# Optimization experiments

Measured on AMD Instinct MI355X. Metric: run time of the kernel, lower is better.

The kernel has to match this reference:

```python
import jax, jax.numpy as jnp
import numpy as np

THRESHOLD = 0.1  # matches init kwarg 'threshold'


def setup_inputs() -> dict:
    key = jax.random.key(0)
    ks = jax.random.split(key, 4)
    B, T, D = 16, 4096, 1024   # batch, tokens(=patch_h*patch_w), d_model
    E, R = 8, 64               # experts, lora rank
    inputs = jax.random.normal(ks[0], (B, T, D), dtype=jnp.float32)
    gate_w = jax.random.normal(ks[1], (D, E), dtype=jnp.float32) * (1.0 / np.sqrt(D))
    gate_b = jnp.zeros((E,), dtype=jnp.float32)
    lora_A = jax.random.normal(ks[2], (E, D, R), dtype=jnp.float32) * (1.0 / np.sqrt(D))
    lora_B = jax.random.normal(ks[3], (E, R, D), dtype=jnp.float32) * (1.0 / np.sqrt(R))
    return {"inputs": inputs, "gate_w": gate_w, "gate_b": gate_b,
            "lora_A": lora_A, "lora_B": lora_B, "patch_h": 64, "patch_w": 64}


def reference(inputs, gate_w, gate_b, lora_A, lora_B, patch_h, patch_w):
    # patch_h / patch_w are unused by 'linear' LoRA experts (kept for signature parity)
    D = inputs.shape[-1]
    x = inputs.reshape(-1, D)                                  # [N, D]
    gate_logits = jax.nn.softmax(x @ gate_w + gate_b, axis=-1)  # [N, E]
    selected = (gate_logits >= THRESHOLD).astype(x.dtype)       # threshold gate
    weights = gate_logits * selected
    wsum = jnp.sum(weights, axis=-1, keepdims=True)
    wsum = jnp.where(wsum == 0, jnp.ones_like(wsum), wsum)
    weights = weights / wsum                                    # renormalized weights [N, E]
    # Dense equivalent of per-expert gather/scatter: tokens with weight 0 contribute nothing,
    # identical to the boolean-indexed accumulation in the torch code.
    h = jnp.einsum('nd,edr->ner', x, lora_A)                    # [N, E, R]
    out = jnp.einsum('ner,erd,ne->nd', h, lora_B, weights)      # weighted combine [N, D]
    return out.reshape(inputs.shape[:-1] + (D,))
```

## Files before the change

kernel.cpp:

```cpp
#include <hip/hip_runtime.h>
#include <stdint.h>
#include <stddef.h>


typedef float f32x4 __attribute__((ext_vector_type(4)));
typedef short bf16x8 __attribute__((ext_vector_type(8)));

#define MFMA_16x16x32(A, B, C) __builtin_amdgcn_mfma_f32_16x16x32_bf16((A), (B), (C), 0, 0, 0)
#define SCHED_FENCE() __builtin_amdgcn_sched_barrier(0)
#define BAR() __builtin_amdgcn_s_barrier()
#define WAIT_LGKM0() asm volatile("s_waitcnt lgkmcnt(0)" ::: "memory")
#define WAIT_VM3() asm volatile("s_waitcnt vmcnt(3)" ::: "memory")
#define WAIT_VM0_LGKM0() asm volatile("s_waitcnt vmcnt(0) lgkmcnt(0)" ::: "memory")
#define WAIT_VM0() asm volatile("s_waitcnt vmcnt(0)" ::: "memory")

__device__ __forceinline__ unsigned short f2bf(float f) {
    union { float f; unsigned int u; } v;
    v.f = f;
    unsigned int u = v.u;
    u += 0x7FFFu + ((u >> 16) & 1u);
    return (unsigned short)(u >> 16);
}

__device__ __forceinline__ void load16_lds(unsigned short* lds, const unsigned short* g) {
    __builtin_amdgcn_global_load_lds(
        (const __attribute__((address_space(1))) unsigned int*)g,
        (__attribute__((address_space(3))) unsigned int*)lds, 16, 0, 0);
}

__global__ __launch_bounds__(256) void convert_pack(
        const float* __restrict__ LA, const float* __restrict__ LB,
        unsigned short* __restrict__ A_P, unsigned short* __restrict__ B_P) {
    int gid = blockIdx.x * 256 + threadIdx.x;
    if (gid < 524288) {
        int j = gid & 7, l = (gid >> 3) & 63, cblk = (gid >> 9) & 31, kblk = gid >> 14;
        int d = kblk * 32 + (l >> 4) * 8 + j;
        int col = cblk * 16 + (l & 15);
        int e = col >> 6, r = col & 63;
        A_P[gid] = f2bf(LA[((size_t)e * 1024 + d) * 64 + r]);
    } else {
        int idx = gid - 524288;
        int j = idx & 7, l = (idx >> 3) & 63, cblk = (idx >> 9) & 63, kblk = idx >> 15;
        int k = kblk * 32 + (l >> 4) * 8 + j;
        int d = cblk * 16 + (l & 15);
        int e = k >> 6, r = k & 63;
        B_P[idx] = f2bf(LB[((size_t)e * 64 + r) * 1024 + d]);
    }
}

__global__ __launch_bounds__(256) void gate_kernel(
        const float* __restrict__ X, const float* __restrict__ GW,
        const float* __restrict__ GB, float* __restrict__ Wg) {
    __shared__ float gwt[8 * 1024];
    int tid = threadIdx.x;

    {
        float r[4][8];
#pragma unroll
        for (int j = 0; j < 4; ++j) {
            const f32x4* gp = (const f32x4*)(GW + (size_t)(tid * 4 + j) * 8);
            f32x4 g0 = gp[0], g1 = gp[1];
#pragma unroll
            for (int q = 0; q < 4; ++q) { r[j][q] = g0[q]; r[j][4 + q] = g1[q]; }
        }
#pragma unroll
        for (int e = 0; e < 8; ++e) {
            f32x4 v;
#pragma unroll
            for (int j = 0; j < 4; ++j) v[j] = r[j][e];
            *(f32x4*)&gwt[e * 1024 + tid * 4] = v;
        }
    }
    __syncthreads();

    int tg = tid >> 4;
    int sub = tid & 15;
    size_t tok0 = (size_t)blockIdx.x * 64 + tg * 4;
    const float* xr = X + tok0 * 1024 + sub * 4;

    float lg[4][8];
#pragma unroll
    for (int ti = 0; ti < 4; ++ti)
#pragma unroll
        for (int e = 0; e < 8; ++e) lg[ti][e] = 0.f;

#pragma unroll 2
    for (int it = 0; it < 16; ++it) {
        f32x4 g[8];
#pragma unroll
        for (int e = 0; e < 8; ++e)
            g[e] = *(const f32x4*)&gwt[e * 1024 + it * 64 + sub * 4];
#pragma unroll
        for (int ti = 0; ti < 4; ++ti) {
            f32x4 x = *(const f32x4*)(xr + (size_t)ti * 1024 + it * 64);
#pragma unroll
            for (int e = 0; e < 8; ++e) {
                lg[ti][e] += x[0] * g[e][0];
                lg[ti][e] += x[1] * g[e][1];
                lg[ti][e] += x[2] * g[e][2];
                lg[ti][e] += x[3] * g[e][3];
            }
        }
    }
#pragma unroll
    for (int s = 1; s < 16; s <<= 1) {
#pragma unroll
        for (int ti = 0; ti < 4; ++ti)
#pragma unroll
            for (int e = 0; e < 8; ++e)
                lg[ti][e] += __shfl_xor(lg[ti][e], s, 16);
    }
#pragma unroll
    for (int ti = 0; ti < 4; ++ti) {
        float p[8], m = -1e30f, ssum = 0.f, l2[8];
#pragma unroll
        for (int e = 0; e < 8; ++e) { l2[e] = lg[ti][e] + GB[e]; m = fmaxf(m, l2[e]); }
#pragma unroll
        for (int e = 0; e < 8; ++e) { p[e] = expf(l2[e] - m); ssum += p[e]; }
        float inv = 1.f / ssum;
        float wv[8], wsum = 0.f;
#pragma unroll
        for (int e = 0; e < 8; ++e) {
            float pe = p[e] * inv;
            wv[e] = (pe >= 0.1f) ? pe : 0.f;
            wsum += wv[e];
        }
        if (wsum == 0.f) wsum = 1.f;
        float invw = 1.f / wsum;
        if (sub < 8) Wg[(tok0 + ti) * 8 + sub] = wv[sub] * invw;
    }
}

__global__ __launch_bounds__(512, 4) void stage1_kernel(
        const float* __restrict__ X, const unsigned short* __restrict__ A_P,
        const float* __restrict__ Wg, unsigned short* __restrict__ H_P) {
    __shared__ union SM1 {
        struct {
            unsigned short a[2][32 * 512];
            unsigned short x[2][64 * 40];
        } p;
        unsigned short hb[64 * 520];
    } sm;
    __shared__ float wl[512];

    int tid = threadIdx.x;
    int lane = tid & 63;
    int w = tid >> 6;
    int blk = blockIdx.x;
    int row = tid >> 3;
    int sub = tid & 7;

    wl[tid] = Wg[(size_t)blk * 512 + tid];

    const float* xp = X + (size_t)blk * 64 * 1024 + (size_t)row * 1024 + sub * 4;
    unsigned short* aCur = sm.p.a[0];
    unsigned short* aNxt = sm.p.a[1];
    unsigned short* xCur = sm.p.x[0];
    unsigned short* xNxt = sm.p.x[1];

    {
        const unsigned short* asrc = A_P + tid * 8;
#pragma unroll
        for (int i = 0; i < 4; ++i)
            load16_lds(&aCur[tid * 8 + i * 4096], asrc + i * 4096);
    }
    SCHED_FENCE();
    f32x4 xv0 = *(const f32x4*)(xp);
    f32x4 xv_hold = *(const f32x4*)(xp + 32);
    {
        unsigned int lo = (unsigned int)f2bf(xv0[0]) | ((unsigned int)f2bf(xv0[1]) << 16);
        unsigned int hi = (unsigned int)f2bf(xv0[2]) | ((unsigned int)f2bf(xv0[3]) << 16);
        *((uint2*)&xCur[row * 40 + sub * 4]) = make_uint2(lo, hi);
    }

    f32x4 acc[4][4] = {};
    for (int kb = 0; kb < 31; ++kb) {
        const unsigned short* asrc = A_P + (size_t)(kb + 1) * 16384 + tid * 8;
#pragma unroll
        for (int i = 0; i < 4; ++i)
            load16_lds(&aNxt[tid * 8 + i * 4096], asrc + i * 4096);
        SCHED_FENCE();
        int kbn = (kb + 2 <= 31) ? kb + 2 : 31;
        f32x4 xv_new = *(const f32x4*)(xp + (size_t)kbn * 32);
        unsigned int lo = (unsigned int)f2bf(xv_hold[0]) | ((unsigned int)f2bf(xv_hold[1]) << 16);
        unsigned int hi = (unsigned int)f2bf(xv_hold[2]) | ((unsigned int)f2bf(xv_hold[3]) << 16);
        *((uint2*)&xNxt[row * 40 + sub * 4]) = make_uint2(lo, hi);
        WAIT_LGKM0();
        SCHED_FENCE();
        BAR();
        SCHED_FENCE();
        bf16x8 af[4], bv[4];
#pragma unroll
        for (int m = 0; m < 4; ++m)
            af[m] = *(const bf16x8*)&xCur[(m * 16 + (lane & 15)) * 40 + (lane >> 4) * 8];
#pragma unroll
        for (int n = 0; n < 4; ++n)
            bv[n] = *(const bf16x8*)&aCur[(w * 4 + n) * 512 + lane * 8];
#pragma unroll
        for (int m = 0; m < 4; ++m)
#pragma unroll
            for (int n = 0; n < 4; ++n)
                acc[m][n] = MFMA_16x16x32(af[m], bv[n], acc[m][n]);
        BAR();
        unsigned short* t;
        t = aCur; aCur = aNxt; aNxt = t;
        t = xCur; xCur = xNxt; xNxt = t;
        xv_hold = xv_new;
    }
    WAIT_VM0_LGKM0();
    SCHED_FENCE();
    BAR();
    SCHED_FENCE();
    {
        bf16x8 af[4], bv[4];
#pragma unroll
        for (int m = 0; m < 4; ++m)
            af[m] = *(const bf16x8*)&xCur[(m * 16 + (lane & 15)) * 40 + (lane >> 4) * 8];
#pragma unroll
        for (int n = 0; n < 4; ++n)
            bv[n] = *(const bf16x8*)&aCur[(w * 4 + n) * 512 + lane * 8];
#pragma unroll
        for (int m = 0; m < 4; ++m)
#pragma unroll
            for (int n = 0; n < 4; ++n)
                acc[m][n] = MFMA_16x16x32(af[m], bv[n], acc[m][n]);
    }
    __syncthreads();

#pragma unroll
    for (int m = 0; m < 4; ++m) {
        float wv[4];
#pragma unroll
        for (int r = 0; r < 4; ++r)
            wv[r] = wl[(m * 16 + (lane >> 4) * 4 + r) * 8 + w];
#pragma unroll
        for (int n = 0; n < 4; ++n) {
            int col = w * 64 + n * 16 + (lane & 15);
#pragma unroll
            for (int r = 0; r < 4; ++r) {
                int rr = m * 16 + (lane >> 4) * 4 + r;
                sm.hb[rr * 520 + col] = f2bf(acc[m][n][r] * wv[r]);
            }
        }
    }
    __syncthreads();
#pragma unroll
    for (int it = 0; it < 8; ++it) {
        int gi = tid + it * 512;
        int ft = gi >> 6;
        int l2 = gi & 63;
        int rowblk = ft >> 4;
        int kblk = ft & 15;
        int rr = rowblk * 16 + (l2 & 15);
        int cs = kblk * 32 + (l2 >> 4) * 8;
        uint4 v = *(const uint4*)&sm.hb[rr * 520 + cs];
        *(uint4*)&H_P[(((size_t)blk * 4 + rowblk) * 16 + kblk) * 512 + l2 * 8] = v;
    }
}

__global__ __launch_bounds__(512, 4) void stage2_kernel(
        const unsigned short* __restrict__ H_P, const unsigned short* __restrict__ B_P,
        float* __restrict__ Out) {
    __shared__ unsigned short a_lds[2][8 * 512];
    __shared__ unsigned short b_lds[2][16 * 512];

    int tid = threadIdx.x;
    int lane = tid & 63;
    int wid = tid >> 6;
    int wr = wid >> 2, wc = wid & 3;
    int bw = blockIdx.x;
    int mt = ((bw >> 5) << 3) | (bw & 7);
    int nt = (bw >> 3) & 3;

    unsigned short* aCur = a_lds[0];
    unsigned short* aNxt = a_lds[1];
    unsigned short* bCur = b_lds[0];
    unsigned short* bNxt = b_lds[1];

    const unsigned short* hbase = H_P + ((size_t)mt * 8 + wid) * 16 * 512 + lane * 8;
    const unsigned short* bbase = B_P + (size_t)nt * 16 * 512 + tid * 8;

    load16_lds(&aCur[tid * 8], hbase);
    load16_lds(&bCur[tid * 8], bbase);
    load16_lds(&bCur[tid * 8 + 4096], bbase + 4096);

    f32x4 acc[4][4] = {};
    for (int kc = 0; kc < 15; ++kc) {
        load16_lds(&aNxt[tid * 8], hbase + (size_t)(kc + 1) * 512);
        load16_lds(&bNxt[tid * 8], bbase + (size_t)(kc + 1) * 32768);
        load16_lds(&bNxt[tid * 8 + 4096], bbase + (size_t)(kc + 1) * 32768 + 4096);
        WAIT_VM3();
        SCHED_FENCE();
        BAR();
        SCHED_FENCE();
        bf16x8 af[4], bv[4];
#pragma unroll
        for (int m = 0; m < 4; ++m)
            af[m] = *(const bf16x8*)&aCur[(wr * 4 + m) * 512 + lane * 8];
#pragma unroll
        for (int n = 0; n < 4; ++n)
            bv[n] = *(const bf16x8*)&bCur[(wc * 4 + n) * 512 + lane * 8];
#pragma unroll
        for (int m = 0; m < 4; ++m)
#pragma unroll
            for (int n = 0; n < 4; ++n)
                acc[m][n] = MFMA_16x16x32(af[m], bv[n], acc[m][n]);
        BAR();
        unsigned short* t;
        t = aCur; aCur = aNxt; aNxt = t;
        t = bCur; bCur = bNxt; bNxt = t;
    }
    WAIT_VM0();
    SCHED_FENCE();
    BAR();
    SCHED_FENCE();
    {
        bf16x8 af[4], bv[4];
#pragma unroll
        for (int m = 0; m < 4; ++m)
            af[m] = *(const bf16x8*)&aCur[(wr * 4 + m) * 512 + lane * 8];
#pragma unroll
        for (int n = 0; n < 4; ++n)
            bv[n] = *(const bf16x8*)&bCur[(wc * 4 + n) * 512 + lane * 8];
#pragma unroll
        for (int m = 0; m < 4; ++m)
#pragma unroll
            for (int n = 0; n < 4; ++n)
                acc[m][n] = MFMA_16x16x32(af[m], bv[n], acc[m][n]);
    }

    size_t rb = (size_t)mt * 128 + wr * 64;
    int cb = nt * 256 + wc * 64;
#pragma unroll
    for (int m = 0; m < 4; ++m)
#pragma unroll
        for (int n = 0; n < 4; ++n) {
            int col = cb + n * 16 + (lane & 15);
#pragma unroll
            for (int r = 0; r < 4; ++r) {
                size_t rrow = rb + m * 16 + (lane >> 4) * 4 + r;
                Out[rrow * 1024 + col] = acc[m][n][r];
            }
        }
}

extern "C" void kernel_launch(void* const* d_in, const int* in_sizes, int n_in,
                              void* d_out, int out_size, void* d_ws, size_t ws_size,
                              hipStream_t stream) {
    const float* X  = (const float*)d_in[0];
    const float* GW = (const float*)d_in[1];
    const float* GB = (const float*)d_in[2];
    const float* LA = (const float*)d_in[3];
    const float* LB = (const float*)d_in[4];
    float* Out = (float*)d_out;

    char* ws = (char*)d_ws;
    float*          Wg  = (float*)ws;
    unsigned short* A_P = (unsigned short*)(ws + (2u << 20));
    unsigned short* B_P = (unsigned short*)(ws + (3u << 20));
    unsigned short* H_P = (unsigned short*)(ws + (4u << 20));

    convert_pack<<<4096, 256, 0, stream>>>(LA, LB, A_P, B_P);
    gate_kernel<<<1024, 256, 0, stream>>>(X, GW, GB, Wg);
    stage1_kernel<<<1024, 512, 0, stream>>>(X, A_P, Wg, H_P);
    stage2_kernel<<<2048, 512, 0, stream>>>(H_P, B_P, Out);
}
```

Baseline: 308.6 us.

## Merge weight packing and gate into one launch with prefetched token rows

Combines the LoRA weight bf16 conversion/packing kernel and the gating kernel into a single launch, using a block-index split: blocks at index 2048 and above pack the weights, and the lower blocks compute the gate. This removes one kernel launch and lets the two independent jobs run side by side on the GPU. The gate part now handles 2 tokens per 16-lane group instead of 4, doubling the gate grid, and keeps x rows in registers with a software prefetch of the second half. The trade-off is higher register pressure, plus packing blocks that reserve the gate's LDS allocation.

```diff
diff --git a/kernel.cpp b/kernel.cpp
--- a/kernel.cpp
+++ b/kernel.cpp
@@ -28,32 +28,33 @@
         (__attribute__((address_space(3))) unsigned int*)lds, 16, 0, 0);
 }
 
-__global__ __launch_bounds__(256) void convert_pack(
+__global__ __launch_bounds__(256) void gate_pack_kernel(
+        const float* __restrict__ X, const float* __restrict__ GW,
+        const float* __restrict__ GB, float* __restrict__ Wg,
         const float* __restrict__ LA, const float* __restrict__ LB,
         unsigned short* __restrict__ A_P, unsigned short* __restrict__ B_P) {
-    int gid = blockIdx.x * 256 + threadIdx.x;
-    if (gid < 524288) {
-        int j = gid & 7, l = (gid >> 3) & 63, cblk = (gid >> 9) & 31, kblk = gid >> 14;
-        int d = kblk * 32 + (l >> 4) * 8 + j;
-        int col = cblk * 16 + (l & 15);
-        int e = col >> 6, r = col & 63;
-        A_P[gid] = f2bf(LA[((size_t)e * 1024 + d) * 64 + r]);
-    } else {
-        int idx = gid - 524288;
-        int j = idx & 7, l = (idx >> 3) & 63, cblk = (idx >> 9) & 63, kblk = idx >> 15;
-        int k = kblk * 32 + (l >> 4) * 8 + j;
-        int d = cblk * 16 + (l & 15);
-        int e = k >> 6, r = k & 63;
-        B_P[idx] = f2bf(LB[((size_t)e * 64 + r) * 1024 + d]);
-    }
-}
-
-__global__ __launch_bounds__(256) void gate_kernel(
-        const float* __restrict__ X, const float* __restrict__ GW,
-        const float* __restrict__ GB, float* __restrict__ Wg) {
+    int tid = threadIdx.x;
+
+    if (blockIdx.x >= 2048) {
+        int gid = (blockIdx.x - 2048) * 256 + tid;
+        if (gid < 524288) {
+            int j = gid & 7, l = (gid >> 3) & 63, cblk = (gid >> 9) & 31, kblk = gid >> 14;
+            int d = kblk * 32 + (l >> 4) * 8 + j;
+            int col = cblk * 16 + (l & 15);
+            int e = col >> 6, r = col & 63;
+            A_P[gid] = f2bf(LA[((size_t)e * 1024 + d) * 64 + r]);
+        } else {
+            int idx = gid - 524288;
+            int j = idx & 7, l = (idx >> 3) & 63, cblk = (idx >> 9) & 63, kblk = idx >> 15;
+            int k = kblk * 32 + (l >> 4) * 8 + j;
+            int d = cblk * 16 + (l & 15);
+            int e = k >> 6, r = k & 63;
+            B_P[idx] = f2bf(LB[((size_t)e * 64 + r) * 1024 + d]);
+        }
+        return;
+    }
+
     __shared__ float gwt[8 * 1024];
-    int tid = threadIdx.x;
-
     {
         float r[4][8];
 #pragma unroll
@@ -73,45 +74,57 @@
     }
     __syncthreads();
 
-    int tg = tid >> 4;
+    int grp = tid >> 4;
     int sub = tid & 15;
-    size_t tok0 = (size_t)blockIdx.x * 64 + tg * 4;
-    const float* xr = X + tok0 * 1024 + sub * 4;
-
-    float lg[4][8];
-#pragma unroll
-    for (int ti = 0; ti < 4; ++ti)
-#pragma unroll
-        for (int e = 0; e < 8; ++e) lg[ti][e] = 0.f;
-
-#pragma unroll 2
+    size_t t0 = (size_t)blockIdx.x * 32 + grp * 2;
+    const float* xr0 = X + t0 * 1024 + sub * 4;
+    const float* xr1 = xr0 + 1024;
+
+    f32x4 xsA[8], xsB[8];
+#pragma unroll
+    for (int i = 0; i < 8; ++i) {
+        xsA[i] = *(const f32x4*)(xr0 + i * 64);
+        xsB[i] = *(const f32x4*)(xr1 + i * 64);
+    }
+
+    float lg[2][8];
+#pragma unroll
+    for (int e = 0; e < 8; ++e) { lg[0][e] = 0.f; lg[1][e] = 0.f; }
+
+#pragma unroll
     for (int it = 0; it < 16; ++it) {
         f32x4 g[8];
 #pragma unroll
         for (int e = 0; e < 8; ++e)
             g[e] = *(const f32x4*)&gwt[e * 1024 + it * 64 + sub * 4];
-#pragma unroll
-        for (int ti = 0; ti < 4; ++ti) {
-            f32x4 x = *(const f32x4*)(xr + (size_t)ti * 1024 + it * 64);
-#pragma unroll
-            for (int e = 0; e < 8; ++e) {
-                lg[ti][e] += x[0] * g[e][0];
-                lg[ti][e] += x[1] * g[e][1];
-                lg[ti][e] += x[2] * g[e][2];
-                lg[ti][e] += x[3] * g[e][3];
-            }
+        f32x4 xa = xsA[it & 7];
+        f32x4 xb = xsB[it & 7];
+        if (it < 8) {
+            xsA[it & 7] = *(const f32x4*)(xr0 + (it + 8) * 64);
+            xsB[it & 7] = *(const f32x4*)(xr1 + (it + 8) * 64);
+        }
+#pragma unroll
+        for (int e = 0; e < 8; ++e) {
+            lg[0][e] += xa[0] * g[e][0];
+            lg[0][e] += xa[1] * g[e][1];
+            lg[0][e] += xa[2] * g[e][2];
+            lg[0][e] += xa[3] * g[e][3];
+            lg[1][e] += xb[0] * g[e][0];
+            lg[1][e] += xb[1] * g[e][1];
+            lg[1][e] += xb[2] * g[e][2];
+            lg[1][e] += xb[3] * g[e][3];
         }
     }
 #pragma unroll
     for (int s = 1; s < 16; s <<= 1) {
 #pragma unroll
-        for (int ti = 0; ti < 4; ++ti)
+        for (int ti = 0; ti < 2; ++ti)
 #pragma unroll
             for (int e = 0; e < 8; ++e)
                 lg[ti][e] += __shfl_xor(lg[ti][e], s, 16);
     }
 #pragma unroll
-    for (int ti = 0; ti < 4; ++ti) {
+    for (int ti = 0; ti < 2; ++ti) {
         float p[8], m = -1e30f, ssum = 0.f, l2[8];
 #pragma unroll
         for (int e = 0; e < 8; ++e) { l2[e] = lg[ti][e] + GB[e]; m = fmaxf(m, l2[e]); }
@@ -127,7 +140,7 @@
         }
         if (wsum == 0.f) wsum = 1.f;
         float invw = 1.f / wsum;
-        if (sub < 8) Wg[(tok0 + ti) * 8 + sub] = wv[sub] * invw;
+        if (sub < 8) Wg[(t0 + ti) * 8 + sub] = wv[sub] * invw;
     }
 }
 
@@ -360,8 +373,7 @@
     unsigned short* B_P = (unsigned short*)(ws + (3u << 20));
     unsigned short* H_P = (unsigned short*)(ws + (4u << 20));
 
-    convert_pack<<<4096, 256, 0, stream>>>(LA, LB, A_P, B_P);
-    gate_kernel<<<1024, 256, 0, stream>>>(X, GW, GB, Wg);
+    gate_pack_kernel<<<6144, 256, 0, stream>>>(X, GW, GB, Wg, LA, LB, A_P, B_P);
     stage1_kernel<<<1024, 512, 0, stream>>>(X, A_P, Wg, H_P);
     stage2_kernel<<<2048, 512, 0, stream>>>(H_P, B_P, Out);
 }
```

Result: faster. 282.1 us (-8.6%).
